# Performance work log

Measured on AMD Instinct MI355X. Metric: run time of the kernel, lower is better.

## Reference

```python
import jax, jax.numpy as jnp
import numpy as np
import math

B, H, M, L, D = 4, 8, 512, 2048, 64   # batch, heads, block len, span, head dim
RAMP = 64                              # adapt_span_len (soft-mask ramp size)


def setup_inputs() -> dict:
    key = jax.random.key(0)
    ks = jax.random.split(key, 5)
    BH = B * H
    KL = M + L
    return {
        "query": jax.random.normal(ks[0], (BH, M, D), jnp.float32),
        "key_": jax.random.normal(ks[1], (BH, KL, D), jnp.float32),
        "value": jax.random.normal(ks[2], (BH, KL, D), jnp.float32),
        "key_pe": jax.random.normal(ks[3], (1, D, L), jnp.float32) * 0.02,
        "current_val": jax.random.uniform(ks[4], (H, 1, 1), jnp.float32, minval=0.3, maxval=0.9),
    }


def reference(query, key_, value, key_pe, current_val):
    BH, Mq, Dh = query.shape
    KL = key_.shape[1]
    Lw = KL - Mq  # attention span
    nb = BH // current_val.shape[0]  # batch size (heads folded into leading dim)

    # full scores then unskew: band[b, i, j] = scores[b, i, i + j]
    scores = jnp.einsum('bmd,bnd->bmn', query, key_)              # (BH, M, M+L)
    rows = jnp.arange(Mq)[:, None]                                # (M, 1)
    band_idx = rows + jnp.arange(Lw)[None, :]                     # (M, L)
    attn = scores[:, rows, band_idx]                              # (BH, M, L)

    # relative position bias, scale, softmax
    attn = attn + jnp.einsum('bmd,dl->bml', query, key_pe[0])
    attn = attn / math.sqrt(Dh)
    attn = jax.nn.softmax(attn, axis=-1)

    # adaptive span soft mask (per head) + renormalization
    template = jnp.arange(1 - Lw, 1, dtype=attn.dtype)            # (L,) = linspace(1-L, 0, L)
    mask = jnp.clip((template + current_val * Lw) / RAMP + 1.0, 0.0, 1.0)  # (H, 1, L)
    attn4 = attn.reshape(nb, -1, Mq, Lw) * mask[None]             # (B, H, M, L)
    attn4 = attn4 / (attn4.sum(-1, keepdims=True) + 1e-8)
    attn = attn4.reshape(BH, Mq, Lw)

    # skew back to (BH, M, M+L) and contract with values
    skewed = jnp.zeros((BH, Mq, KL), attn.dtype).at[:, rows, band_idx].set(attn)
    out = jnp.einsum('bmn,bnd->bmd', skewed, value)               # (BH, M, D)
    return out
```

## Files before the change

### kernel.cpp

```cpp
#include <hip/hip_runtime.h>

typedef _Float16 half_t;
typedef _Float16 half8 __attribute__((ext_vector_type(8)));
typedef _Float16 half4 __attribute__((ext_vector_type(4)));
typedef _Float16 half2v __attribute__((ext_vector_type(2)));
typedef float f32x4 __attribute__((ext_vector_type(4)));
typedef float f32x16 __attribute__((ext_vector_type(16)));
typedef unsigned int uint4v __attribute__((ext_vector_type(4)));

#define MFMA_S(a, b, c) __builtin_amdgcn_mfma_f32_32x32x16_f16((a), (b), (c), 0, 0, 0)

static constexpr int kM  = 512;
static constexpr int kD  = 64;
static constexpr int kKL = 2560;
static constexpr int kL  = 2048;
static constexpr int WS_QS  = 0;
static constexpr int WS_KB  = 1048576;
static constexpr int WS_VC  = WS_KB + 5242880;
static constexpr int WS_PET = WS_VC + 5242880;
static constexpr int WS_Z   = WS_PET + 131072;

__global__ __launch_bounds__(256) void prep_kernel(const float* __restrict__ q,
    const float* __restrict__ k, const float* __restrict__ v,
    const float* __restrict__ pe, half_t* __restrict__ ws, float* __restrict__ out) {
  __shared__ float ls[64 * 72];
  const int b = blockIdx.x, t = threadIdx.x;
  if (b < 3072) {
    const int i = b * 256 + t;
    const float QS = 0.125f * 1.4426950408889634f;
    const float* src; half_t* dst; float sc;
    if (i < 131072) { src = q + (size_t)i * 8; dst = ws + WS_QS + (size_t)i * 8; sc = QS; }
    else { const int j = i - 131072; src = k + (size_t)j * 8; dst = ws + WS_KB + (size_t)j * 8; sc = 1.0f; }
    const float4 a = ((const float4*)src)[0];
    const float4 bb = ((const float4*)src)[1];
    half_t tt[8];
    tt[0] = (half_t)(a.x * sc);  tt[1] = (half_t)(a.y * sc);
    tt[2] = (half_t)(a.z * sc);  tt[3] = (half_t)(a.w * sc);
    tt[4] = (half_t)(bb.x * sc); tt[5] = (half_t)(bb.y * sc);
    tt[6] = (half_t)(bb.z * sc); tt[7] = (half_t)(bb.w * sc);
    *(int4*)dst = *(int4*)tt;
    return;
  }
  if (b >= 4384) {
    if (b < 4640) {
      float4* o = (float4*)out;
      const int base = (b - 4384) * 1024 + t;
#pragma unroll
      for (int u = 0; u < 4; ++u) o[base + u * 256] = float4{0, 0, 0, 0};
    } else {
      float4* z = (float4*)((float*)(ws + WS_Z));
      const int base = (b - 4640) * 1024 + t;
#pragma unroll
      for (int u = 0; u < 4; ++u) z[base + u * 256] = float4{0, 0, 0, 0};
    }
    return;
  }
  const bool isV = (b < 4352);
  int bh = 0, kt = 0, b3 = 0;
  const float* src; int sstride;
  if (isV) {
    const int b2 = b - 3072;
    bh = b2 / 40; kt = b2 % 40;
    src = v + (size_t)(bh * 2560 + kt * 64) * 64; sstride = 64;
  } else {
    b3 = b - 4352;
    src = pe + (size_t)b3 * 64; sstride = 2048;
  }
  const int rr = t >> 4, cq = (t & 15) * 4;
#pragma unroll
  for (int p = 0; p < 4; ++p) {
    const float4 x = *(const float4*)(src + (size_t)(p * 16 + rr) * sstride + cq);
    *(float4*)(ls + (p * 16 + rr) * 72 + cq) = x;
  }
  __syncthreads();
  const int oc = t >> 2, ch = t & 3;
  half_t tmp[16];
#pragma unroll
  for (int i2 = 0; i2 < 16; ++i2) tmp[i2] = (half_t)ls[(ch * 16 + i2) * 72 + oc];
  half_t* o;
  if (isV) {
    o = ws + WS_VC + (size_t)bh * 163840 + ((kt << 1) + (ch >> 1)) * 2048 + oc * 32 + ((ch & 1) << 4);
  } else {
    o = ws + WS_PET + ((size_t)b3 * 64 + oc) * 64 + ch * 16;
  }
  ((int4*)o)[0] = ((int4*)tmp)[0];
  ((int4*)o)[1] = ((int4*)tmp)[1];
}

__global__ __launch_bounds__(256, 4) void attn_kernel(
    const half_t* __restrict__ ws, const float* __restrict__ cvp,
    float* __restrict__ out, float* __restrict__ zmA) {

  __shared__ __align__(16) char smem[36864];
  half_t* lsh = (half_t*)smem;

  const int tid  = threadIdx.x;
  const int lane = tid & 63;
  const int w    = tid >> 6;
  const int c32  = lane & 31;
  const int h    = lane >> 5;

  const int id = blockIdx.x;
  const int bh = ((id & 7) << 2) | (id >> 8);
  const int mid = (id >> 3) & 31;
  const int mb = mid & 3, sp = mid >> 2;
  const int m0 = mb << 7;
  const int g0 = (sp << 3) + (sp < 4 ? sp : 4);
  const int cnt = (sp < 4) ? 9 : 8;

  const float cvl = cvp[bh & 7] * 2048.0f - 2047.0f;
  const float cvO = cvl * 0.015625f + 1.0f;

  const half_t* kb  = ws + WS_KB + (size_t)bh * (kKL * kD);
  const half_t* vcb = ws + WS_VC + (size_t)bh * (kKL * kD);
  const half_t* pet = ws + WS_PET;

  const half_t* qrow = ws + WS_QS + (size_t)(bh * kM + m0 + 32 * w + c32) * kD;
  half8 bq[4];
#pragma unroll
  for (int t = 0; t < 4; ++t) bq[t] = *(const half8*)(qrow + t * 16 + h * 8);

  half_t* stf = lsh + 9728 + w * 2176 + c32 * 68;

  int4 stgK, stgV;
  auto issueKV = [&](int gg) {
    const int r = tid >> 3, seg = tid & 7;
    const int krow = m0 + (gg << 5) + r;
    stgK = *(const int4*)(kb + (size_t)krow * kD + seg * 8);
    const int vch = (m0 >> 5) + gg;
    stgV = *(const int4*)(vcb + (size_t)vch * 2048 + tid * 8);
  };
  auto commitKV = [&](int gg) {
    const int sK = (gg & 1) * 2304;
    const int sV = 4608 + (gg & 1) * 2560;
    const int r = tid >> 3, seg = tid & 7;
    *(int4*)(lsh + sK + r * 72 + seg * 8) = stgK;
    const int d = tid >> 2, ks = (tid & 3) * 8;
    *(int4*)(lsh + sV + d * 40 + ks) = stgV;
  };

  auto peWindow = [&](int wb) -> f32x16 {
    int l = wb + c32; l = l < 0 ? 0 : (l > kL - 1 ? kL - 1 : l);
    const half_t* pp = pet + (size_t)l * kD;
    f32x16 a = {};
#pragma unroll
    for (int t = 0; t < 4; ++t) {
      const half8 p = *(const half8*)(pp + t * 16 + h * 8);
      a = MFMA_S(p, bq[t], a);
    }
    return a;
  };
  auto stripWrite = [&](int wb, const f32x16& a) {
    const int allone  = (wb >= 0) && (wb + 31 <= kL - 1) && (wb + cvl >= 0.0f);
    const int allzero = (wb > kL - 1) || (wb + 31 < 0) || ((float)(wb + 31) + cvl <= -64.0f);
#pragma unroll
    for (int reg = 0; reg < 16; ++reg) {
      const int lr = (reg & 3) + 8 * (reg >> 2) + 4 * h;
      const int l  = wb + lr;
      const float bt = a[reg] * 0.6931472f;
      float e = __builtin_fmaf(bt, 0.16666667f, 0.5f);
      e = __builtin_fmaf(e, bt, 1.0f);
      e = __builtin_fmaf(e, bt, 1.0f);
      float em;
      if (allzero) em = 0.0f;
      else if (allone) em = e;
      else {
        const float mk = fminf(fmaxf((float)l * 0.015625f + cvO, 0.0f), 1.0f);
        em = ((unsigned)l < (unsigned)kL) ? e * mk : 0.0f;
      }
      stf[(l + c32) & 63] = (half_t)em;
    }
  };

  issueKV(g0);
  const int B0 = (g0 << 5) - 32 * w;
  stripWrite(B0 - 32, peWindow(B0 - 32));
  stripWrite(B0,      peWindow(B0));
  commitKV(g0);
  __syncthreads();

  float zmc = 0.0f;
  f32x16 o0 = {}, o1 = {};

  for (int t = 0; t < cnt; ++t) {
    const int g = g0 + t;
    const bool more = (t + 1 < cnt);
    if (more) issueKV(g + 1);

    const int sK = (g & 1) * 2304;
    const int sV = 4608 + (g & 1) * 2560;
    const int B = (g << 5) - 32 * w;

    half8 ak[4];
#pragma unroll
    for (int kt = 0; kt < 4; ++kt)
      ak[kt] = *(const half8*)(lsh + sK + c32 * 72 + kt * 16 + h * 8);

    half4 emq[4];
#pragma unroll
    for (int q = 0; q < 4; ++q)
      emq[q] = *(const half4*)(stf + ((B + 8 * q + 4 * h) & 63));

    half8 av[2][2];
#pragma unroll
    for (int dh = 0; dh < 2; ++dh)
#pragma unroll
      for (int kt = 0; kt < 2; ++kt)
        av[dh][kt] = *(const half8*)(lsh + sV + (32 * dh + c32) * 40 + kt * 16 + h * 8);

    f32x16 s = {};
#pragma unroll
    for (int kt = 0; kt < 4; ++kt) s = MFMA_S(ak[kt], bq[kt], s);

    float pm[16];
#pragma unroll
    for (int reg = 0; reg < 16; ++reg) {
      pm[reg] = __builtin_amdgcn_exp2f(s[reg]) * (float)emq[reg >> 2][reg & 3];
      zmc += pm[reg];
    }
    unsigned Wp[8];
#pragma unroll
    for (int q = 0; q < 8; ++q) {
      const half2v hp = { (half_t)pm[2 * q], (half_t)pm[2 * q + 1] };
      Wp[q] = __builtin_bit_cast(unsigned, hp);
    }
    const auto r0 = __builtin_amdgcn_permlane32_swap(Wp[0], Wp[2], false, false);
    const auto r1 = __builtin_amdgcn_permlane32_swap(Wp[1], Wp[3], false, false);
    const auto r2 = __builtin_amdgcn_permlane32_swap(Wp[4], Wp[6], false, false);
    const auto r3 = __builtin_amdgcn_permlane32_swap(Wp[5], Wp[7], false, false);
    const uint4v u0 = { (unsigned)r0[0], (unsigned)r1[0], (unsigned)r0[1], (unsigned)r1[1] };
    const uint4v u1 = { (unsigned)r2[0], (unsigned)r3[0], (unsigned)r2[1], (unsigned)r3[1] };
    const half8 pb0 = __builtin_bit_cast(half8, u0);
    const half8 pb1 = __builtin_bit_cast(half8, u1);

    o0 = MFMA_S(av[0][0], pb0, o0);
    o0 = MFMA_S(av[0][1], pb1, o0);
    o1 = MFMA_S(av[1][0], pb0, o1);
    o1 = MFMA_S(av[1][1], pb1, o1);

    if (more) {
      stripWrite(B + 32, peWindow(B + 32));
      commitKV(g + 1);
    }
    __syncthreads();
  }

  __syncthreads();
  float* Ow = (float*)smem + (size_t)w * 2176;
#pragma unroll
  for (int q = 0; q < 4; ++q) {
    *(f32x4*)(Ow + c32 * 68 + 0  + 8 * q + 4 * h) =
        f32x4{o0[q * 4], o0[q * 4 + 1], o0[q * 4 + 2], o0[q * 4 + 3]};
    *(f32x4*)(Ow + c32 * 68 + 32 + 8 * q + 4 * h) =
        f32x4{o1[q * 4], o1[q * 4 + 1], o1[q * 4 + 2], o1[q * 4 + 3]};
  }
  zmc += __shfl_xor(zmc, 32);
  if (lane < 32) {
    const int row = bh * kM + m0 + 32 * w + c32;
    atomicAdd(&zmA[row], zmc);
  }
  const int rowbase = bh * kM + m0 + 32 * w;
  for (int rr = 0; rr < 32; ++rr)
    atomicAdd(out + (size_t)(rowbase + rr) * kD + lane, Ow[rr * 68 + lane]);
}

__global__ __launch_bounds__(256) void norm_kernel(const float* __restrict__ zmA,
    float* __restrict__ out) {
  const int i = blockIdx.x * 256 + threadIdx.x;
  const int row = i >> 4, d4 = (i & 15) << 2;
  const float inv = 1.0f / (zmA[row] + 1e-20f);
  float4* p = (float4*)(out + (size_t)row * 64 + d4);
  float4 v = *p;
  v.x *= inv; v.y *= inv; v.z *= inv; v.w *= inv;
  *p = v;
}

extern "C" void kernel_launch(void* const* d_in, const int* in_sizes, int n_in,
                              void* d_out, int out_size, void* d_ws, size_t ws_size,
                              hipStream_t stream) {
  (void)in_sizes; (void)n_in; (void)out_size; (void)ws_size;
  const float* q  = (const float*)d_in[0];
  const float* k  = (const float*)d_in[1];
  const float* v  = (const float*)d_in[2];
  const float* pe = (const float*)d_in[3];
  const float* cv = (const float*)d_in[4];
  half_t* ws = (half_t*)d_ws;
  float* out = (float*)d_out;
  float* zmA = (float*)(ws + WS_Z);

  prep_kernel<<<4648, 256, 0, stream>>>(q, k, v, pe, ws, out);
  attn_kernel<<<1024, 256, 0, stream>>>(ws, cv, out, zmA);
  norm_kernel<<<1024, 256, 0, stream>>>(zmA, out);
}
```

Before: 143.3 us.

## Replace atomic split-span reduction with per-split partial buffers and log-domain mask

Splits the key span into 4 equal chunks of 17 tiles instead of 8 uneven chunks, halving the grid to 512 blocks. Each block writes its partial output and row sum to a dedicated workspace slice, and the norm kernel sums the four partials, so the atomics and the zero-fill pass in prep go away. The position-bias and mask factor is stored as a log-domain additive term, which replaces a multiply with an add inside exp2. It also relaxes launch bounds to 2 blocks per SM. The risk is lower parallelism from fewer blocks, plus extra partial-buffer traffic.

```diff
diff --git a/kernel.cpp b/kernel.cpp
--- a/kernel.cpp
+++ b/kernel.cpp
@@ -1,4 +1,5 @@
 #include <hip/hip_runtime.h>
+#include <math.h>
 
 typedef _Float16 half_t;
 typedef _Float16 half8 __attribute__((ext_vector_type(8)));
@@ -18,11 +19,12 @@
 static constexpr int WS_KB  = 1048576;
 static constexpr int WS_VC  = WS_KB + 5242880;
 static constexpr int WS_PET = WS_VC + 5242880;
-static constexpr int WS_Z   = WS_PET + 131072;
+static constexpr size_t WS_ZP_B = 23330816;
+static constexpr size_t WS_PO_B = WS_ZP_B + 262144;
 
 __global__ __launch_bounds__(256) void prep_kernel(const float* __restrict__ q,
     const float* __restrict__ k, const float* __restrict__ v,
-    const float* __restrict__ pe, half_t* __restrict__ ws, float* __restrict__ out) {
+    const float* __restrict__ pe, half_t* __restrict__ ws) {
   __shared__ float ls[64 * 72];
   const int b = blockIdx.x, t = threadIdx.x;
   if (b < 3072) {
@@ -41,20 +43,6 @@
     *(int4*)dst = *(int4*)tt;
     return;
   }
-  if (b >= 4384) {
-    if (b < 4640) {
-      float4* o = (float4*)out;
-      const int base = (b - 4384) * 1024 + t;
-#pragma unroll
-      for (int u = 0; u < 4; ++u) o[base + u * 256] = float4{0, 0, 0, 0};
-    } else {
-      float4* z = (float4*)((float*)(ws + WS_Z));
-      const int base = (b - 4640) * 1024 + t;
-#pragma unroll
-      for (int u = 0; u < 4; ++u) z[base + u * 256] = float4{0, 0, 0, 0};
-    }
-    return;
-  }
   const bool isV = (b < 4352);
   int bh = 0, kt = 0, b3 = 0;
   const float* src; int sstride;
@@ -87,9 +75,9 @@
   ((int4*)o)[1] = ((int4*)tmp)[1];
 }
 
-__global__ __launch_bounds__(256, 4) void attn_kernel(
+__global__ __launch_bounds__(256, 2) void attn_kernel(
     const half_t* __restrict__ ws, const float* __restrict__ cvp,
-    float* __restrict__ out, float* __restrict__ zmA) {
+    float* __restrict__ po, float* __restrict__ zp) {
 
   __shared__ __align__(16) char smem[36864];
   half_t* lsh = (half_t*)smem;
@@ -101,12 +89,11 @@
   const int h    = lane >> 5;
 
   const int id = blockIdx.x;
-  const int bh = ((id & 7) << 2) | (id >> 8);
-  const int mid = (id >> 3) & 31;
+  const int bh = ((id & 7) << 2) | (id >> 7);
+  const int mid = (id >> 3) & 15;
   const int mb = mid & 3, sp = mid >> 2;
   const int m0 = mb << 7;
-  const int g0 = (sp << 3) + (sp < 4 ? sp : 4);
-  const int cnt = (sp < 4) ? 9 : 8;
+  const int g0 = sp * 17;
 
   const float cvl = cvp[bh & 7] * 2048.0f - 2047.0f;
   const float cvO = cvl * 0.015625f + 1.0f;
@@ -157,18 +144,15 @@
     for (int reg = 0; reg < 16; ++reg) {
       const int lr = (reg & 3) + 8 * (reg >> 2) + 4 * h;
       const int l  = wb + lr;
-      const float bt = a[reg] * 0.6931472f;
-      float e = __builtin_fmaf(bt, 0.16666667f, 0.5f);
-      e = __builtin_fmaf(e, bt, 1.0f);
-      e = __builtin_fmaf(e, bt, 1.0f);
-      float em;
-      if (allzero) em = 0.0f;
-      else if (allone) em = e;
+      float bl;
+      if (allzero) bl = -HUGE_VALF;
+      else if (allone) bl = a[reg];
       else {
         const float mk = fminf(fmaxf((float)l * 0.015625f + cvO, 0.0f), 1.0f);
-        em = ((unsigned)l < (unsigned)kL) ? e * mk : 0.0f;
+        const float lg = __builtin_amdgcn_logf(mk);
+        bl = ((unsigned)l < (unsigned)kL) ? a[reg] + lg : -HUGE_VALF;
       }
-      stf[(l + c32) & 63] = (half_t)em;
+      stf[(l + c32) & 63] = (half_t)bl;
     }
   };
 
@@ -182,9 +166,9 @@
   float zmc = 0.0f;
   f32x16 o0 = {}, o1 = {};
 
-  for (int t = 0; t < cnt; ++t) {
+  for (int t = 0; t < 17; ++t) {
     const int g = g0 + t;
-    const bool more = (t + 1 < cnt);
+    const bool more = (t < 16);
     if (more) issueKV(g + 1);
 
     const int sK = (g & 1) * 2304;
@@ -215,7 +199,7 @@
     float pm[16];
 #pragma unroll
     for (int reg = 0; reg < 16; ++reg) {
-      pm[reg] = __builtin_amdgcn_exp2f(s[reg]) * (float)emq[reg >> 2][reg & 3];
+      pm[reg] = __builtin_amdgcn_exp2f(s[reg] + (float)emq[reg >> 2][reg & 3]);
       zmc += pm[reg];
     }
     unsigned Wp[8];
@@ -245,7 +229,6 @@
     __syncthreads();
   }
 
-  __syncthreads();
   float* Ow = (float*)smem + (size_t)w * 2176;
 #pragma unroll
   for (int q = 0; q < 4; ++q) {
@@ -255,24 +238,29 @@
         f32x4{o1[q * 4], o1[q * 4 + 1], o1[q * 4 + 2], o1[q * 4 + 3]};
   }
   zmc += __shfl_xor(zmc, 32);
-  if (lane < 32) {
-    const int row = bh * kM + m0 + 32 * w + c32;
-    atomicAdd(&zmA[row], zmc);
-  }
   const int rowbase = bh * kM + m0 + 32 * w;
-  for (int rr = 0; rr < 32; ++rr)
-    atomicAdd(out + (size_t)(rowbase + rr) * kD + lane, Ow[rr * 68 + lane]);
-}
-
-__global__ __launch_bounds__(256) void norm_kernel(const float* __restrict__ zmA,
-    float* __restrict__ out) {
+  if (lane < 32) zp[(size_t)sp * 16384 + rowbase + c32] = zmc;
+  float* pob = po + ((size_t)sp * 16384 + rowbase) * 64;
+#pragma unroll
+  for (int u = 0; u < 8; ++u) {
+    const int row = u * 4 + (lane >> 4);
+    const int d4 = (lane & 15) << 2;
+    *(f32x4*)(pob + (size_t)row * 64 + d4) = *(const f32x4*)(Ow + row * 68 + d4);
+  }
+}
+
+__global__ __launch_bounds__(256) void norm_kernel(const float* __restrict__ zp,
+    const float* __restrict__ po, float* __restrict__ out) {
   const int i = blockIdx.x * 256 + threadIdx.x;
   const int row = i >> 4, d4 = (i & 15) << 2;
-  const float inv = 1.0f / (zmA[row] + 1e-20f);
-  float4* p = (float4*)(out + (size_t)row * 64 + d4);
-  float4 v = *p;
-  v.x *= inv; v.y *= inv; v.z *= inv; v.w *= inv;
-  *p = v;
+  const float z = zp[row] + zp[16384 + row] + zp[32768 + row] + zp[49152 + row];
+  const float inv = 1.0f / (z + 1e-20f);
+  f32x4 a = *(const f32x4*)(po + (size_t)row * 64 + d4);
+  const f32x4 b = *(const f32x4*)(po + 1048576u + (size_t)row * 64 + d4);
+  const f32x4 c = *(const f32x4*)(po + 2097152u + (size_t)row * 64 + d4);
+  const f32x4 d = *(const f32x4*)(po + 3145728u + (size_t)row * 64 + d4);
+  a = a + b + c + d;
+  *(f32x4*)(out + (size_t)row * 64 + d4) = a * inv;
 }
 
 extern "C" void kernel_launch(void* const* d_in, const int* in_sizes, int n_in,
@@ -286,9 +274,10 @@
   const float* cv = (const float*)d_in[4];
   half_t* ws = (half_t*)d_ws;
   float* out = (float*)d_out;
-  float* zmA = (float*)(ws + WS_Z);
-
-  prep_kernel<<<4648, 256, 0, stream>>>(q, k, v, pe, ws, out);
-  attn_kernel<<<1024, 256, 0, stream>>>(ws, cv, out, zmA);
-  norm_kernel<<<1024, 256, 0, stream>>>(zmA, out);
-}
+  float* zp = (float*)((char*)d_ws + WS_ZP_B);
+  float* po = (float*)((char*)d_ws + WS_PO_B);
+
+  prep_kernel<<<4384, 256, 0, stream>>>(q, k, v, pe, ws);
+  attn_kernel<<<512, 256, 0, stream>>>(ws, cv, po, zp);
+  norm_kernel<<<1024, 256, 0, stream>>>(zp, po, out);
+}
```

Result: faster. 134.5 us (-6.1%).
